# Kernel optimization log

Measured on AMD Instinct MI355X. Metric: run time of the kernel, lower is better.

The kernel has to match this reference:

```python
import jax, jax.numpy as jnp
import numpy as np

N = 131072      # total sentences
D = 512         # d_MLP_size == bag_feature_dim
D_ATT = 256
N_HEAD = 4
N_CLASSES = 53
BAG_SIZE = 16
N_BAGS = N // BAG_SIZE


def setup_inputs() -> dict:
    key = jax.random.key(0)
    k_x, k_w1, k_w2, k_wc, k_bc = jax.random.split(key, 5)
    x = jax.random.normal(k_x, (N, D), dtype=jnp.float32)
    # equal-sized bags (ragged boundaries collapsed to segment ids)
    seg_ids = (jnp.arange(N, dtype=jnp.int32) // BAG_SIZE).astype(jnp.int32)
    # parameters, stored (in, out); math identical to nn.Linear(x @ W.T)
    W1 = jax.random.normal(k_w1, (D, D_ATT), dtype=jnp.float32) / np.sqrt(D)
    W2 = jax.random.normal(k_w2, (D_ATT, N_HEAD), dtype=jnp.float32) / np.sqrt(D_ATT)
    Wc = jax.random.normal(k_wc, (D, N_CLASSES), dtype=jnp.float32) / np.sqrt(D)
    bc = jax.random.normal(k_bc, (N_CLASSES,), dtype=jnp.float32) * 0.01
    return {"x": x, "W1": W1, "W2": W2, "Wc": Wc, "bc": bc,
            "seg_ids": seg_ids, "n_bags": N_BAGS}


def reference(x, W1, W2, Wc, bc, seg_ids, n_bags):
    # scores per sentence per head: tanh(x W1) W2  -> (N, H)
    s = jnp.tanh(x @ W1) @ W2
    # segment-wise (per-bag) softmax over sentences, per head
    smax = jax.ops.segment_max(s, seg_ids, num_segments=n_bags)      # (B, H)
    e = jnp.exp(s - smax[seg_ids])                                   # (N, H)
    denom = jax.ops.segment_sum(e, seg_ids, num_segments=n_bags)     # (B, H)
    alpha = e / denom[seg_ids]                                       # (N, H)
    # torch: mean over heads of (H, n_i) attention, then alpha @ x
    w = jnp.mean(alpha, axis=1)                                      # (N,)
    bag_repr = jax.ops.segment_sum(w[:, None] * x, seg_ids,
                                   num_segments=n_bags)              # (B, D)
    # dropout is identity in eval / p=0
    logits = bag_repr @ Wc + bc                                      # (B, C)
    return logits
```

## Files before the change

kernel.cpp:

```cpp
#include <hip/hip_runtime.h>
#include <hip/hip_bf16.h>

#define N_TOTAL   131072
#define D         512
#define D_ATT     256
#define N_HEAD    4
#define N_CLASSES 53
#define BAG       16
#define M_TILE    64
#define BAGS_PER_BLK (M_TILE / BAG)
#define THREADS   256
#define N_BLOCKS  (N_TOTAL / M_TILE)

typedef __attribute__((ext_vector_type(8))) short bf16x8;
typedef __attribute__((ext_vector_type(4))) float f32x4;

__device__ __forceinline__ unsigned short f2bf(float f) {
    __hip_bfloat16 h = __float2bfloat16(f);
    return *reinterpret_cast<unsigned short*>(&h);
}
__device__ __forceinline__ float bfbits2f(unsigned int lo16) {
    return __uint_as_float(lo16 << 16);
}
__device__ __forceinline__ float bfhi2f(unsigned int hibits) {
    return __uint_as_float(hibits & 0xffff0000u);
}

__global__ void prep_kernel(const float* __restrict__ W1, const float* __restrict__ Wc,
                            unsigned short* __restrict__ W1T, float* __restrict__ WcT) {
    int tid = blockIdx.x * 256 + threadIdx.x;
    if (tid < D * D_ATT) {
        int k = tid >> 8;
        int n = tid & 255;
        W1T[n * D + k] = f2bf(W1[k * D_ATT + n]);
    } else {
        int t2 = tid - D * D_ATT;
        if (t2 < D * N_CLASSES) {
            int k = t2 / N_CLASSES;
            int c = t2 - k * N_CLASSES;
            WcT[c * D + k] = Wc[k * N_CLASSES + c];
        }
    }
}

#define LDX 520
#define LDH 260
#define LDR 516

__global__ void __launch_bounds__(THREADS)
fused_kernel(const float* __restrict__ x,
             const unsigned short* __restrict__ W1T,
             const float* __restrict__ W2,
             const float* __restrict__ WcT,
             const float* __restrict__ bc,
             float* __restrict__ out)
{
    __shared__ __align__(16) unsigned char lds_u[66560];
    __shared__ float ldsW2T[N_HEAD * D_ATT];
    __shared__ float ldsS[M_TILE * N_HEAD];
    __shared__ float ldsM[BAGS_PER_BLK * N_HEAD];
    __shared__ float ldsDen[BAGS_PER_BLK * N_HEAD];
    __shared__ float ldsW[M_TILE];

    unsigned short* ldsX = (unsigned short*)lds_u;
    unsigned short* ldsH = (unsigned short*)lds_u;
    float*          ldsR = (float*)(lds_u + 33280);

    const int tid  = threadIdx.x;
    const int wave = tid >> 6;
    const int lane = tid & 63;
    const int quad = lane >> 4;
    const int l16  = lane & 15;
    const int wc2  = wave * 64;
    const int row_base = blockIdx.x * M_TILE;

    for (int i = tid; i < D_ATT * N_HEAD; i += THREADS) {
        int n = i >> 2, h = i & 3;
        ldsW2T[h * D_ATT + n] = W2[i];
    }

    {
        const float* xb = &x[(size_t)row_base * D];
        #pragma unroll 8
        for (int i = 0; i < 32; ++i) {
            int f  = i * THREADS + tid;
            int r  = f >> 7;
            int c4 = f & 127;
            float4 v = *reinterpret_cast<const float4*>(&xb[(size_t)r * D + c4 * 4]);
            unsigned int p0 = (unsigned int)f2bf(v.x) | ((unsigned int)f2bf(v.y) << 16);
            unsigned int p1 = (unsigned int)f2bf(v.z) | ((unsigned int)f2bf(v.w) << 16);
            uint2 p; p.x = p0; p.y = p1;
            *reinterpret_cast<uint2*>(&ldsX[r * LDX + c4 * 4]) = p;
        }
    }
    __syncthreads();

    f32x4 acc[4][4] = {};
    {
        const unsigned short* Wb = &W1T[(size_t)wc2 * D];
        bf16x8 a0[4], b0[4], a1[4], b1[4];

        #define LOAD_A(ks, dst)                                                        \
            { int kb = (ks) * 32 + quad * 8;                                           \
              _Pragma("unroll")                                                        \
              for (int mi = 0; mi < 4; ++mi)                                           \
                  dst[mi] = *reinterpret_cast<const bf16x8*>(                          \
                      &ldsX[(mi * 16 + l16) * LDX + kb]); }
        #define LOAD_B(ks, dst)                                                        \
            { int kb = (ks) * 32 + quad * 8;                                           \
              _Pragma("unroll")                                                        \
              for (int ni = 0; ni < 4; ++ni)                                           \
                  dst[ni] = *reinterpret_cast<const bf16x8*>(                          \
                      &Wb[(size_t)(ni * 16 + l16) * D + kb]); }
        #define MFMA(af, bfr)                                                          \
            { _Pragma("unroll")                                                        \
              for (int mi = 0; mi < 4; ++mi)                                           \
                  _Pragma("unroll")                                                    \
                  for (int ni = 0; ni < 4; ++ni)                                       \
                      acc[mi][ni] = __builtin_amdgcn_mfma_f32_16x16x32_bf16(           \
                          af[mi], bfr[ni], acc[mi][ni], 0, 0, 0); }

        LOAD_A(0, a0); LOAD_B(0, b0);
        #pragma unroll
        for (int ks = 0; ks < 16; ks += 2) {
            LOAD_A(ks + 1, a1); LOAD_B(ks + 1, b1);
            MFMA(a0, b0);
            if (ks + 2 < 16) { LOAD_A(ks + 2, a0); LOAD_B(ks + 2, b0); }
            MFMA(a1, b1);
        }
        #undef LOAD_A
        #undef LOAD_B
        #undef MFMA
    }
    __syncthreads();

    #pragma unroll
    for (int mi = 0; mi < 4; ++mi) {
        #pragma unroll
        for (int ni = 0; ni < 4; ++ni) {
            f32x4 v = acc[mi][ni];
            #pragma unroll
            for (int r = 0; r < 4; ++r) {
                float e = __expf(2.f * v[r]);
                float t = 1.f - 2.f / (e + 1.f);
                int row = mi * 16 + quad * 4 + r;
                int col = wc2 + ni * 16 + l16;
                ldsH[row * LDH + col] = f2bf(t);
            }
        }
    }
    __syncthreads();

    {
        const int row  = tid >> 2;
        const int head = tid & 3;
        const unsigned short* hrow = &ldsH[row * LDH];
        const float* w2h = &ldsW2T[head * D_ATT];
        float s = 0.f;
        #pragma unroll 8
        for (int j = 0; j < 64; ++j) {
            uint2 u = *reinterpret_cast<const uint2*>(&hrow[j * 4]);
            float4 wv = *reinterpret_cast<const float4*>(&w2h[j * 4]);
            s += bfbits2f(u.x & 0xffffu) * wv.x + bfhi2f(u.x) * wv.y
               + bfbits2f(u.y & 0xffffu) * wv.z + bfhi2f(u.y) * wv.w;
        }
        ldsS[row * 4 + head] = s;
    }
    __syncthreads();

    if (tid < BAGS_PER_BLK * N_HEAD) {
        int bag = tid >> 2, head = tid & 3;
        float m = -1e30f;
        for (int i = 0; i < BAG; ++i)
            m = fmaxf(m, ldsS[(bag * BAG + i) * 4 + head]);
        float den = 0.f;
        for (int i = 0; i < BAG; ++i)
            den += __expf(ldsS[(bag * BAG + i) * 4 + head] - m);
        ldsM[tid] = m;
        ldsDen[tid] = 1.f / den;
    }
    __syncthreads();
    if (tid < M_TILE) {
        int row = tid, bag = row >> 4;
        float w = 0.f;
        #pragma unroll
        for (int h = 0; h < 4; ++h)
            w += __expf(ldsS[row * 4 + h] - ldsM[bag * 4 + h]) * ldsDen[bag * 4 + h];
        ldsW[row] = 0.25f * w;
    }
    __syncthreads();

    {
        const int b  = wave;
        const int dc = lane * 8;
        float4 r0 = {0.f, 0.f, 0.f, 0.f}, r1 = {0.f, 0.f, 0.f, 0.f};
        for (int i = 0; i < BAG; ++i) {
            int row = b * BAG + i;
            float wv = ldsW[row];
            const float4* xp = reinterpret_cast<const float4*>(
                &x[(size_t)(row_base + row) * D + dc]);
            float4 a = xp[0], c = xp[1];
            r0.x += wv * a.x; r0.y += wv * a.y; r0.z += wv * a.z; r0.w += wv * a.w;
            r1.x += wv * c.x; r1.y += wv * c.y; r1.z += wv * c.z; r1.w += wv * c.w;
        }
        *reinterpret_cast<float4*>(&ldsR[b * LDR + dc])     = r0;
        *reinterpret_cast<float4*>(&ldsR[b * LDR + dc + 4]) = r1;
    }
    __syncthreads();

    {
        int c = tid >> 2;
        int b = tid & 3;
        if (c < N_CLASSES) {
            float a = bc[c];
            const float4* rp = reinterpret_cast<const float4*>(&ldsR[b * LDR]);
            const float4* wp = reinterpret_cast<const float4*>(&WcT[(size_t)c * D]);
            #pragma unroll 8
            for (int j = 0; j < D / 4; ++j) {
                float4 r = rp[j], w = wp[j];
                a += r.x * w.x + r.y * w.y + r.z * w.z + r.w * w.w;
            }
            out[((size_t)blockIdx.x * BAGS_PER_BLK + b) * N_CLASSES + c] = a;
        }
    }
}

extern "C" void kernel_launch(void* const* d_in, const int* in_sizes, int n_in,
                              void* d_out, int out_size, void* d_ws, size_t ws_size,
                              hipStream_t stream) {
    const float* x  = (const float*)d_in[0];
    const float* W1 = (const float*)d_in[1];
    const float* W2 = (const float*)d_in[2];
    const float* Wc = (const float*)d_in[3];
    const float* bc = (const float*)d_in[4];

    unsigned short* W1T = (unsigned short*)d_ws;
    float*          WcT = (float*)((char*)d_ws + (size_t)D * D_ATT * 2);

    int prep_total = D * D_ATT + D * N_CLASSES;
    prep_kernel<<<dim3((prep_total + 255) / 256), dim3(256), 0, stream>>>(W1, Wc, W1T, WcT);

    fused_kernel<<<dim3(N_BLOCKS), dim3(THREADS), 0, stream>>>(
        x, W1T, W2, WcT, bc, (float*)d_out);
}
```

Before: 476.4 us.

## Stream x directly from global into MFMA fragments and fuse tanh-W2 in registers

```diff
diff --git a/kernel.cpp b/kernel.cpp
--- a/kernel.cpp
+++ b/kernel.cpp
@@ -19,11 +19,10 @@
     __hip_bfloat16 h = __float2bfloat16(f);
     return *reinterpret_cast<unsigned short*>(&h);
 }
-__device__ __forceinline__ float bfbits2f(unsigned int lo16) {
-    return __uint_as_float(lo16 << 16);
-}
-__device__ __forceinline__ float bfhi2f(unsigned int hibits) {
-    return __uint_as_float(hibits & 0xffff0000u);
+__device__ __forceinline__ unsigned int pack_bf(float a, float b) {
+    unsigned int ua = __float_as_uint(a) + 0x8000u;
+    unsigned int ub = __float_as_uint(b) + 0x8000u;
+    return __builtin_amdgcn_perm(ub, ua, 0x07060302u);
 }
 
 __global__ void prep_kernel(const float* __restrict__ W1, const float* __restrict__ Wc,
@@ -43,11 +42,9 @@
     }
 }
 
-#define LDX 520
-#define LDH 260
 #define LDR 516
 
-__global__ void __launch_bounds__(THREADS)
+__global__ void __launch_bounds__(THREADS, 3)
 fused_kernel(const float* __restrict__ x,
              const unsigned short* __restrict__ W1T,
              const float* __restrict__ W2,
@@ -55,16 +52,12 @@
              const float* __restrict__ bc,
              float* __restrict__ out)
 {
-    __shared__ __align__(16) unsigned char lds_u[66560];
-    __shared__ float ldsW2T[N_HEAD * D_ATT];
+    __shared__ float ldsSp[4][M_TILE][N_HEAD];
     __shared__ float ldsS[M_TILE * N_HEAD];
     __shared__ float ldsM[BAGS_PER_BLK * N_HEAD];
     __shared__ float ldsDen[BAGS_PER_BLK * N_HEAD];
     __shared__ float ldsW[M_TILE];
-
-    unsigned short* ldsX = (unsigned short*)lds_u;
-    unsigned short* ldsH = (unsigned short*)lds_u;
-    float*          ldsR = (float*)(lds_u + 33280);
+    __shared__ __align__(16) float ldsR[BAGS_PER_BLK][LDR];
 
     const int tid  = threadIdx.x;
     const int wave = tid >> 6;
@@ -74,97 +67,100 @@
     const int wc2  = wave * 64;
     const int row_base = blockIdx.x * M_TILE;
 
-    for (int i = tid; i < D_ATT * N_HEAD; i += THREADS) {
-        int n = i >> 2, h = i & 3;
-        ldsW2T[h * D_ATT + n] = W2[i];
-    }
-
-    {
-        const float* xb = &x[(size_t)row_base * D];
-        #pragma unroll 8
-        for (int i = 0; i < 32; ++i) {
-            int f  = i * THREADS + tid;
-            int r  = f >> 7;
-            int c4 = f & 127;
-            float4 v = *reinterpret_cast<const float4*>(&xb[(size_t)r * D + c4 * 4]);
-            unsigned int p0 = (unsigned int)f2bf(v.x) | ((unsigned int)f2bf(v.y) << 16);
-            unsigned int p1 = (unsigned int)f2bf(v.z) | ((unsigned int)f2bf(v.w) << 16);
-            uint2 p; p.x = p0; p.y = p1;
-            *reinterpret_cast<uint2*>(&ldsX[r * LDX + c4 * 4]) = p;
-        }
-    }
-    __syncthreads();
+    const float*          pA = x + (size_t)row_base * D + (size_t)l16 * D + quad * 8;
+    const unsigned short* pB = W1T + (size_t)(wc2 + l16) * D + quad * 8;
 
     f32x4 acc[4][4] = {};
     {
-        const unsigned short* Wb = &W1T[(size_t)wc2 * D];
-        bf16x8 a0[4], b0[4], a1[4], b1[4];
-
-        #define LOAD_A(ks, dst)                                                        \
-            { int kb = (ks) * 32 + quad * 8;                                           \
-              _Pragma("unroll")                                                        \
-              for (int mi = 0; mi < 4; ++mi)                                           \
-                  dst[mi] = *reinterpret_cast<const bf16x8*>(                          \
-                      &ldsX[(mi * 16 + l16) * LDX + kb]); }
-        #define LOAD_B(ks, dst)                                                        \
-            { int kb = (ks) * 32 + quad * 8;                                           \
-              _Pragma("unroll")                                                        \
-              for (int ni = 0; ni < 4; ++ni)                                           \
-                  dst[ni] = *reinterpret_cast<const bf16x8*>(                          \
-                      &Wb[(size_t)(ni * 16 + l16) * D + kb]); }
-        #define MFMA(af, bfr)                                                          \
-            { _Pragma("unroll")                                                        \
-              for (int mi = 0; mi < 4; ++mi)                                           \
-                  _Pragma("unroll")                                                    \
-                  for (int ni = 0; ni < 4; ++ni)                                       \
-                      acc[mi][ni] = __builtin_amdgcn_mfma_f32_16x16x32_bf16(           \
-                          af[mi], bfr[ni], acc[mi][ni], 0, 0, 0); }
-
-        LOAD_A(0, a0); LOAD_B(0, b0);
+        float4 ra[4][2], rb[4][2];
+        bf16x8 bfrag[4];
+
+        #define LOADA(ks, dst)                                                          \
+            { _Pragma("unroll")                                                         \
+              for (int mi = 0; mi < 4; ++mi) {                                          \
+                  const float* p = pA + (size_t)mi * 16 * D + (ks) * 32;                \
+                  dst[mi][0] = *reinterpret_cast<const float4*>(p);                     \
+                  dst[mi][1] = *reinterpret_cast<const float4*>(p + 4);                 \
+              } }
+        #define LOADB(ks)                                                               \
+            { _Pragma("unroll")                                                         \
+              for (int ni = 0; ni < 4; ++ni)                                            \
+                  bfrag[ni] = *reinterpret_cast<const bf16x8*>(                         \
+                      pB + (size_t)ni * 16 * D + (ks) * 32); }
+        #define STEP(buf)                                                               \
+            { _Pragma("unroll")                                                         \
+              for (int mi = 0; mi < 4; ++mi) {                                          \
+                  bf16x8 af;                                                            \
+                  unsigned int* afp = reinterpret_cast<unsigned int*>(&af);             \
+                  afp[0] = pack_bf(buf[mi][0].x, buf[mi][0].y);                         \
+                  afp[1] = pack_bf(buf[mi][0].z, buf[mi][0].w);                         \
+                  afp[2] = pack_bf(buf[mi][1].x, buf[mi][1].y);                         \
+                  afp[3] = pack_bf(buf[mi][1].z, buf[mi][1].w);                         \
+                  _Pragma("unroll")                                                     \
+                  for (int ni = 0; ni < 4; ++ni)                                        \
+                      acc[mi][ni] = __builtin_amdgcn_mfma_f32_16x16x32_bf16(            \
+                          af, bfrag[ni], acc[mi][ni], 0, 0, 0);                         \
+              } }
+
+        LOADA(0, ra);
         #pragma unroll
         for (int ks = 0; ks < 16; ks += 2) {
-            LOAD_A(ks + 1, a1); LOAD_B(ks + 1, b1);
-            MFMA(a0, b0);
-            if (ks + 2 < 16) { LOAD_A(ks + 2, a0); LOAD_B(ks + 2, b0); }
-            MFMA(a1, b1);
-        }
-        #undef LOAD_A
-        #undef LOAD_B
-        #undef MFMA
-    }
-    __syncthreads();
-
-    #pragma unroll
-    for (int mi = 0; mi < 4; ++mi) {
-        #pragma unroll
-        for (int ni = 0; ni < 4; ++ni) {
-            f32x4 v = acc[mi][ni];
+            LOADB(ks);
+            LOADA(ks + 1, rb);
+            STEP(ra);
+            LOADB(ks + 1);
+            if (ks + 2 < 16) LOADA(ks + 2, ra);
+            STEP(rb);
+        }
+        #undef LOADA
+        #undef LOADB
+        #undef STEP
+    }
+
+    {
+        float4 w2r[4];
+        #pragma unroll
+        for (int ni = 0; ni < 4; ++ni)
+            w2r[ni] = *reinterpret_cast<const float4*>(&W2[(wc2 + ni * 16 + l16) * 4]);
+
+        #pragma unroll
+        for (int mi = 0; mi < 4; ++mi) {
+            float sp[4][4] = {};
             #pragma unroll
-            for (int r = 0; r < 4; ++r) {
-                float e = __expf(2.f * v[r]);
-                float t = 1.f - 2.f / (e + 1.f);
-                int row = mi * 16 + quad * 4 + r;
-                int col = wc2 + ni * 16 + l16;
-                ldsH[row * LDH + col] = f2bf(t);
+            for (int ni = 0; ni < 4; ++ni) {
+                f32x4 v = acc[mi][ni];
+                #pragma unroll
+                for (int r = 0; r < 4; ++r) {
+                    float e = __expf(2.f * v[r]);
+                    float t = 1.f - 2.f / (e + 1.f);
+                    sp[r][0] += t * w2r[ni].x;
+                    sp[r][1] += t * w2r[ni].y;
+                    sp[r][2] += t * w2r[ni].z;
+                    sp[r][3] += t * w2r[ni].w;
+                }
             }
-        }
-    }
-    __syncthreads();
-
-    {
-        const int row  = tid >> 2;
-        const int head = tid & 3;
-        const unsigned short* hrow = &ldsH[row * LDH];
-        const float* w2h = &ldsW2T[head * D_ATT];
-        float s = 0.f;
-        #pragma unroll 8
-        for (int j = 0; j < 64; ++j) {
-            uint2 u = *reinterpret_cast<const uint2*>(&hrow[j * 4]);
-            float4 wv = *reinterpret_cast<const float4*>(&w2h[j * 4]);
-            s += bfbits2f(u.x & 0xffffu) * wv.x + bfhi2f(u.x) * wv.y
-               + bfbits2f(u.y & 0xffffu) * wv.z + bfhi2f(u.y) * wv.w;
-        }
-        ldsS[row * 4 + head] = s;
+            #pragma unroll
+            for (int m = 1; m < 16; m <<= 1)
+                #pragma unroll
+                for (int r = 0; r < 4; ++r)
+                    #pragma unroll
+                    for (int h = 0; h < 4; ++h)
+                        sp[r][h] += __shfl_xor(sp[r][h], m, 64);
+            if (l16 == 0) {
+                #pragma unroll
+                for (int r = 0; r < 4; ++r) {
+                    float4 v4 = {sp[r][0], sp[r][1], sp[r][2], sp[r][3]};
+                    *reinterpret_cast<float4*>(&ldsSp[wave][mi * 16 + quad * 4 + r][0]) = v4;
+                }
+            }
+        }
+    }
+    __syncthreads();
+
+    {
+        int row = tid >> 2, h = tid & 3;
+        float s = ldsSp[0][row][h] + ldsSp[1][row][h] + ldsSp[2][row][h] + ldsSp[3][row][h];
+        ldsS[row * 4 + h] = s;
     }
     __syncthreads();
 
@@ -203,24 +199,29 @@
             r0.x += wv * a.x; r0.y += wv * a.y; r0.z += wv * a.z; r0.w += wv * a.w;
             r1.x += wv * c.x; r1.y += wv * c.y; r1.z += wv * c.z; r1.w += wv * c.w;
         }
-        *reinterpret_cast<float4*>(&ldsR[b * LDR + dc])     = r0;
-        *reinterpret_cast<float4*>(&ldsR[b * LDR + dc + 4]) = r1;
-    }
-    __syncthreads();
-
-    {
-        int c = tid >> 2;
-        int b = tid & 3;
+        *reinterpret_cast<float4*>(&ldsR[b][dc])     = r0;
+        *reinterpret_cast<float4*>(&ldsR[b][dc + 4]) = r1;
+    }
+    __syncthreads();
+
+    {
+        int c = tid >> 1, half = tid & 1;
         if (c < N_CLASSES) {
-            float a = bc[c];
-            const float4* rp = reinterpret_cast<const float4*>(&ldsR[b * LDR]);
-            const float4* wp = reinterpret_cast<const float4*>(&WcT[(size_t)c * D]);
+            int b0 = half * 2, b1 = half * 2 + 1;
+            float a0 = 0.f, a1 = 0.f;
+            const float4* r0p = reinterpret_cast<const float4*>(&ldsR[b0][0]);
+            const float4* r1p = reinterpret_cast<const float4*>(&ldsR[b1][0]);
+            const float4* wp  = reinterpret_cast<const float4*>(&WcT[(size_t)c * D]);
             #pragma unroll 8
             for (int j = 0; j < D / 4; ++j) {
-                float4 r = rp[j], w = wp[j];
-                a += r.x * w.x + r.y * w.y + r.z * w.z + r.w * w.w;
+                float4 w = wp[j], q0 = r0p[j], q1 = r1p[j];
+                a0 += q0.x * w.x + q0.y * w.y + q0.z * w.z + q0.w * w.w;
+                a1 += q1.x * w.x + q1.y * w.y + q1.z * w.z + q1.w * w.w;
             }
-            out[((size_t)blockIdx.x * BAGS_PER_BLK + b) * N_CLASSES + c] = a;
+            float bias = bc[c];
+            size_t ob = (size_t)blockIdx.x * BAGS_PER_BLK;
+            out[(ob + b0) * N_CLASSES + c] = a0 + bias;
+            out[(ob + b1) * N_CLASSES + c] = a1 + bias;
         }
     }
 }
```

Result: slower. 544.6 us (+14.3%).
